# Kernel tuning notes

Measured on AMD Instinct MI355X. Metric: run time of the kernel, lower is better.

Reference implementation:

```python
import jax, jax.numpy as jnp
import numpy as np

N_NODES = 50000
N_EDGES = 600000
D_FEAT = 128
OUT_DIM = 128


def setup_inputs() -> dict:
    key = jax.random.key(0)
    k1, k2, k3, k4 = jax.random.split(key, 4)
    self_feat = jax.random.normal(k1, (N_NODES, D_FEAT), dtype=jnp.float32)
    nbr_feat = jax.random.normal(k2, (N_EDGES, D_FEAT), dtype=jnp.float32)
    relation_src_indices = jax.random.randint(k3, (N_EDGES,), 0, N_NODES, dtype=jnp.int32)
    # Dense(output_dim, use_bias=False), input dim = 2*D_FEAT due to concat
    W = jax.random.normal(k4, (2 * D_FEAT, OUT_DIM), dtype=jnp.float32) * (1.0 / np.sqrt(2 * D_FEAT))
    return {"self_feat": self_feat, "nbr_feat": nbr_feat,
            "relation_src_indices": relation_src_indices, "W": W}


def reference(self_feat, nbr_feat, relation_src_indices, W):
    num_nodes = self_feat.shape[0]
    # unsorted_segment_mean: sum / count, 0 for empty segments (TF semantics)
    seg_sum = jax.ops.segment_sum(nbr_feat, relation_src_indices, num_segments=num_nodes)
    counts = jax.ops.segment_sum(jnp.ones((nbr_feat.shape[0],), dtype=nbr_feat.dtype),
                                 relation_src_indices, num_segments=num_nodes)
    agg = jnp.where(counts[:, None] > 0, seg_sum / jnp.maximum(counts[:, None], 1.0), 0.0)
    out = jnp.concatenate([self_feat, agg], axis=-1)  # [N, 2*D]
    return out @ W  # [N, OUT_DIM]
```

## Files before the change

### kernel.cpp

```cpp
#include <hip/hip_runtime.h>

#define D 128
#define K2 256
#define CAP 96
#define BM 64

typedef float vfloat4 __attribute__((ext_vector_type(4)));
typedef float f32x4 __attribute__((ext_vector_type(4)));
typedef short bf16x8 __attribute__((ext_vector_type(8)));
typedef unsigned short ushort8 __attribute__((ext_vector_type(8)));
typedef unsigned short ushort4v __attribute__((ext_vector_type(4)));

__device__ __forceinline__ unsigned short f2bf(float f) {
    unsigned int u = __float_as_uint(f);
    u += 0x7fffu + ((u >> 16) & 1u);
    return (unsigned short)(u >> 16);
}
__device__ __forceinline__ float bf2f(unsigned short h) {
    return __uint_as_float((unsigned int)h << 16);
}


__global__ void scatter_hist_kernel(const int* __restrict__ idx, int* __restrict__ cnt,
                                    int* __restrict__ eid, int n) {
    int e = blockIdx.x * 256 + threadIdx.x;
    if (e < n) {
        int node = idx[e];
        int p = atomicAdd(&cnt[node], 1);
        if (p < CAP) eid[(size_t)node * CAP + p] = e;
    }
}


__global__ __launch_bounds__(256) void wsplit_kernel(const float* __restrict__ W,
                                                     unsigned short* __restrict__ wh,
                                                     unsigned short* __restrict__ wl) {
    const int k = threadIdx.x;
    const int n = blockIdx.x;
    float x = W[(size_t)k * D + n];
    unsigned short h = f2bf(x);
    float lo = x - bf2f(h);
    wh[(size_t)n * K2 + k] = h;
    wl[(size_t)n * K2 + k] = f2bf(lo);
}


__global__ __launch_bounds__(256) void fused_kernel(const float* __restrict__ self,
                                                    const float* __restrict__ nbr,
                                                    const int* __restrict__ cnt,
                                                    const int* __restrict__ eid,
                                                    const unsigned short* __restrict__ whT,
                                                    const unsigned short* __restrict__ wlT,
                                                    float* __restrict__ out, int nNodes) {
    __shared__ alignas(16) unsigned short AhAll[BM * D];
    __shared__ alignas(16) unsigned short AlAll[BM * D];
    __shared__ alignas(16) unsigned short AhS[BM * 32];
    __shared__ alignas(16) unsigned short AlS[BM * 32];

    const int t = threadIdx.x;
    const int m_base = blockIdx.x * BM;

    {
        const int w = t >> 6;
        const int l = t & 63;
        const int h = l >> 5;
        const int li = l & 31;
        const vfloat4* __restrict__ rows = (const vfloat4*)nbr;
        for (int i = 0; i < 16; ++i) {
            const int r = w * 16 + i;
            const int node = m_base + r;
            if (node >= nNodes) continue;
            const int c0 = cnt[node];
            const int c = (c0 > CAP) ? CAP : c0;
            const int* __restrict__ eb = eid + (size_t)node * CAP;
            vfloat4 acc = {0.f, 0.f, 0.f, 0.f};
            int j = 0;
            for (; j + 8 <= c; j += 8) {
                int e0 = eb[j + 0 + h];
                int e1 = eb[j + 2 + h];
                int e2 = eb[j + 4 + h];
                int e3 = eb[j + 6 + h];
                vfloat4 v0 = __builtin_nontemporal_load(rows + (size_t)e0 * 32 + li);
                vfloat4 v1 = __builtin_nontemporal_load(rows + (size_t)e1 * 32 + li);
                vfloat4 v2 = __builtin_nontemporal_load(rows + (size_t)e2 * 32 + li);
                vfloat4 v3 = __builtin_nontemporal_load(rows + (size_t)e3 * 32 + li);
                acc += (v0 + v1) + (v2 + v3);
            }
            if (j + 4 <= c) {
                int e0 = eb[j + 0 + h];
                int e1 = eb[j + 2 + h];
                vfloat4 v0 = __builtin_nontemporal_load(rows + (size_t)e0 * 32 + li);
                vfloat4 v1 = __builtin_nontemporal_load(rows + (size_t)e1 * 32 + li);
                acc += v0 + v1;
                j += 4;
            }
            for (; j < c; j += 2) {
                int jj = j + h;
                if (jj < c) {
                    int e = eb[jj];
                    vfloat4 v = __builtin_nontemporal_load(rows + (size_t)e * 32 + li);
                    acc += v;
                }
            }
            acc.x += __shfl_xor(acc.x, 32);
            acc.y += __shfl_xor(acc.y, 32);
            acc.z += __shfl_xor(acc.z, 32);
            acc.w += __shfl_xor(acc.w, 32);
            if (h == 0) {
                float inv = (c > 0) ? 1.0f / (float)c : 0.0f;
                vfloat4 o = acc * inv;
                float vv[4] = {o.x, o.y, o.z, o.w};
                ushort4v hv, lv;
#pragma unroll
                for (int q = 0; q < 4; ++q) {
                    unsigned short hh = f2bf(vv[q]);
                    hv[q] = hh;
                    lv[q] = f2bf(vv[q] - bf2f(hh));
                }
                const int sp = ((li >> 1) ^ (r & 7)) * 8 + (li & 1) * 4;
                *(ushort4v*)&AhAll[r * D + sp] = hv;
                *(ushort4v*)&AlAll[r * D + sp] = lv;
            }
        }
    }
    __syncthreads();

    const int sr = t >> 2;
    const int sq = t & 3;
    const int sp = sq ^ ((sr >> 1) & 3);
    int gr = m_base + sr;
    if (gr >= nNodes) gr = nNodes - 1;

    const int wid = t >> 6;
    const int l = t & 63;
    const int wm = (wid >> 1) << 5;
    const int wn = (wid & 1) << 6;
    const int lr = l & 15;
    const int g = l >> 4;
    const int slot = g ^ ((lr >> 1) & 3);

    f32x4 acc[2][4];
#pragma unroll
    for (int i = 0; i < 2; ++i)
#pragma unroll
        for (int j = 0; j < 4; ++j) acc[i][j] = (f32x4){0.f, 0.f, 0.f, 0.f};

    for (int k0 = 0; k0 < D; k0 += 32) {
        const float* p = self + (size_t)gr * D + k0 + sq * 8;
        vfloat4 v0 = ((const vfloat4*)p)[0];
        vfloat4 v1 = ((const vfloat4*)p)[1];
        float xs[8] = {v0.x, v0.y, v0.z, v0.w, v1.x, v1.y, v1.z, v1.w};
        ushort8 hv, lv;
#pragma unroll
        for (int i = 0; i < 8; ++i) {
            unsigned short hh = f2bf(xs[i]);
            hv[i] = hh;
            lv[i] = f2bf(xs[i] - bf2f(hh));
        }
        *(ushort8*)&AhS[sr * 32 + sp * 8] = hv;
        *(ushort8*)&AlS[sr * 32 + sp * 8] = lv;
        __syncthreads();

        bf16x8 bh[4], bl[4], ah[2], al[2];
#pragma unroll
        for (int nf = 0; nf < 4; ++nf) {
            size_t boff = (size_t)(wn + nf * 16 + lr) * K2 + k0 + g * 8;
            bh[nf] = *(const bf16x8*)(whT + boff);
            bl[nf] = *(const bf16x8*)(wlT + boff);
        }
#pragma unroll
        for (int mf = 0; mf < 2; ++mf) {
            int row = wm + mf * 16 + lr;
            ah[mf] = *(const bf16x8*)&AhS[row * 32 + slot * 8];
            al[mf] = *(const bf16x8*)&AlS[row * 32 + slot * 8];
        }
#pragma unroll
        for (int mf = 0; mf < 2; ++mf)
#pragma unroll
            for (int nf = 0; nf < 4; ++nf)
                acc[mf][nf] = __builtin_amdgcn_mfma_f32_16x16x32_bf16(ah[mf], bh[nf], acc[mf][nf], 0, 0, 0);
#pragma unroll
        for (int mf = 0; mf < 2; ++mf)
#pragma unroll
            for (int nf = 0; nf < 4; ++nf)
                acc[mf][nf] = __builtin_amdgcn_mfma_f32_16x16x32_bf16(ah[mf], bl[nf], acc[mf][nf], 0, 0, 0);
#pragma unroll
        for (int mf = 0; mf < 2; ++mf)
#pragma unroll
            for (int nf = 0; nf < 4; ++nf)
                acc[mf][nf] = __builtin_amdgcn_mfma_f32_16x16x32_bf16(al[mf], bh[nf], acc[mf][nf], 0, 0, 0);
        __syncthreads();
    }

    for (int k0 = D; k0 < K2; k0 += 32) {
        bf16x8 bh[4], bl[4], ah[2], al[2];
#pragma unroll
        for (int nf = 0; nf < 4; ++nf) {
            size_t boff = (size_t)(wn + nf * 16 + lr) * K2 + k0 + g * 8;
            bh[nf] = *(const bf16x8*)(whT + boff);
            bl[nf] = *(const bf16x8*)(wlT + boff);
        }
        const int s_log = ((k0 - D) >> 3) + g;
#pragma unroll
        for (int mf = 0; mf < 2; ++mf) {
            int row = wm + mf * 16 + lr;
            int s_phys = s_log ^ (row & 7);
            ah[mf] = *(const bf16x8*)&AhAll[row * D + s_phys * 8];
            al[mf] = *(const bf16x8*)&AlAll[row * D + s_phys * 8];
        }
#pragma unroll
        for (int mf = 0; mf < 2; ++mf)
#pragma unroll
            for (int nf = 0; nf < 4; ++nf)
                acc[mf][nf] = __builtin_amdgcn_mfma_f32_16x16x32_bf16(ah[mf], bh[nf], acc[mf][nf], 0, 0, 0);
#pragma unroll
        for (int mf = 0; mf < 2; ++mf)
#pragma unroll
            for (int nf = 0; nf < 4; ++nf)
                acc[mf][nf] = __builtin_amdgcn_mfma_f32_16x16x32_bf16(ah[mf], bl[nf], acc[mf][nf], 0, 0, 0);
#pragma unroll
        for (int mf = 0; mf < 2; ++mf)
#pragma unroll
            for (int nf = 0; nf < 4; ++nf)
                acc[mf][nf] = __builtin_amdgcn_mfma_f32_16x16x32_bf16(al[mf], bh[nf], acc[mf][nf], 0, 0, 0);
    }

#pragma unroll
    for (int mf = 0; mf < 2; ++mf) {
#pragma unroll
        for (int rr = 0; rr < 4; ++rr) {
            int m = m_base + wm + mf * 16 + g * 4 + rr;
            if (m < nNodes) {
                float* po = out + (size_t)m * D + wn + lr;
#pragma unroll
                for (int nf = 0; nf < 4; ++nf) po[nf * 16] = acc[mf][nf][rr];
            }
        }
    }
}


extern "C" void kernel_launch(void* const* d_in, const int* in_sizes, int n_in,
                              void* d_out, int out_size, void* d_ws, size_t ws_size,
                              hipStream_t stream) {
    const float* self = (const float*)d_in[0];
    const float* nbr = (const float*)d_in[1];
    const int* idx = (const int*)d_in[2];
    const float* W = (const float*)d_in[3];
    float* out = (float*)d_out;

    const int nNodes = in_sizes[0] / D;
    const int nEdges = in_sizes[2];

    int* cnt = (int*)d_ws;
    int* eid = cnt + nNodes;
    size_t csr_bytes = (size_t)nNodes * (1 + CAP) * sizeof(int);
    csr_bytes = (csr_bytes + 15) & ~(size_t)15;
    unsigned short* whT = (unsigned short*)((char*)d_ws + csr_bytes);
    unsigned short* wlT = whT + (size_t)D * K2;

    hipMemsetAsync(cnt, 0, (size_t)nNodes * sizeof(int), stream);
    wsplit_kernel<<<D, K2, 0, stream>>>(W, whT, wlT);
    scatter_hist_kernel<<<(nEdges + 255) / 256, 256, 0, stream>>>(idx, cnt, eid, nEdges);
    fused_kernel<<<(nNodes + BM - 1) / BM, 256, 0, stream>>>(self, nbr, cnt, eid, whT, wlT,
                                                             out, nNodes);
}
```

Before: 500.9 us.

## Fuse count zeroing into W-split kernel and load self features directly into MFMA registers

Replaces the separate memset with a loop inside the weight-split kernel that zeroes the count array, removing one launch. In the self-feature GEMM phase, each lane now loads its own fp32 self rows from global memory and converts them to bf16 hi/lo fragments in registers. This drops the shared staging buffers and the two barriers per k-step. Self rows are now read redundantly by the two N-halves of warps, and the index load is marked nontemporal.

```diff
diff --git a/kernel.cpp b/kernel.cpp
--- a/kernel.cpp
+++ b/kernel.cpp
@@ -21,20 +21,10 @@
 }
 
 
-__global__ void scatter_hist_kernel(const int* __restrict__ idx, int* __restrict__ cnt,
-                                    int* __restrict__ eid, int n) {
-    int e = blockIdx.x * 256 + threadIdx.x;
-    if (e < n) {
-        int node = idx[e];
-        int p = atomicAdd(&cnt[node], 1);
-        if (p < CAP) eid[(size_t)node * CAP + p] = e;
-    }
-}
-
-
-__global__ __launch_bounds__(256) void wsplit_kernel(const float* __restrict__ W,
-                                                     unsigned short* __restrict__ wh,
-                                                     unsigned short* __restrict__ wl) {
+__global__ __launch_bounds__(256) void prep_kernel(const float* __restrict__ W,
+                                                   unsigned short* __restrict__ wh,
+                                                   unsigned short* __restrict__ wl,
+                                                   int* __restrict__ cnt, int nNodes) {
     const int k = threadIdx.x;
     const int n = blockIdx.x;
     float x = W[(size_t)k * D + n];
@@ -42,6 +32,18 @@
     float lo = x - bf2f(h);
     wh[(size_t)n * K2 + k] = h;
     wl[(size_t)n * K2 + k] = f2bf(lo);
+    for (int i = blockIdx.x * 256 + threadIdx.x; i < nNodes; i += 128 * 256) cnt[i] = 0;
+}
+
+
+__global__ void scatter_hist_kernel(const int* __restrict__ idx, int* __restrict__ cnt,
+                                    int* __restrict__ eid, int n) {
+    int e = blockIdx.x * 256 + threadIdx.x;
+    if (e < n) {
+        int node = __builtin_nontemporal_load(idx + e);
+        int p = atomicAdd(&cnt[node], 1);
+        if (p < CAP) eid[(size_t)node * CAP + p] = e;
+    }
 }
 
 
@@ -54,8 +56,6 @@
                                                     float* __restrict__ out, int nNodes) {
     __shared__ alignas(16) unsigned short AhAll[BM * D];
     __shared__ alignas(16) unsigned short AlAll[BM * D];
-    __shared__ alignas(16) unsigned short AhS[BM * 32];
-    __shared__ alignas(16) unsigned short AlS[BM * 32];
 
     const int t = threadIdx.x;
     const int m_base = blockIdx.x * BM;
@@ -125,19 +125,12 @@
     }
     __syncthreads();
 
-    const int sr = t >> 2;
-    const int sq = t & 3;
-    const int sp = sq ^ ((sr >> 1) & 3);
-    int gr = m_base + sr;
-    if (gr >= nNodes) gr = nNodes - 1;
-
     const int wid = t >> 6;
     const int l = t & 63;
     const int wm = (wid >> 1) << 5;
     const int wn = (wid & 1) << 6;
     const int lr = l & 15;
     const int g = l >> 4;
-    const int slot = g ^ ((lr >> 1) & 3);
 
     f32x4 acc[2][4];
 #pragma unroll
@@ -145,22 +138,15 @@
 #pragma unroll
         for (int j = 0; j < 4; ++j) acc[i][j] = (f32x4){0.f, 0.f, 0.f, 0.f};
 
+    const float* selfRow[2];
+#pragma unroll
+    for (int mf = 0; mf < 2; ++mf) {
+        int row = m_base + wm + mf * 16 + lr;
+        if (row >= nNodes) row = nNodes - 1;
+        selfRow[mf] = self + (size_t)row * D + g * 8;
+    }
+
     for (int k0 = 0; k0 < D; k0 += 32) {
-        const float* p = self + (size_t)gr * D + k0 + sq * 8;
-        vfloat4 v0 = ((const vfloat4*)p)[0];
-        vfloat4 v1 = ((const vfloat4*)p)[1];
-        float xs[8] = {v0.x, v0.y, v0.z, v0.w, v1.x, v1.y, v1.z, v1.w};
-        ushort8 hv, lv;
-#pragma unroll
-        for (int i = 0; i < 8; ++i) {
-            unsigned short hh = f2bf(xs[i]);
-            hv[i] = hh;
-            lv[i] = f2bf(xs[i] - bf2f(hh));
-        }
-        *(ushort8*)&AhS[sr * 32 + sp * 8] = hv;
-        *(ushort8*)&AlS[sr * 32 + sp * 8] = lv;
-        __syncthreads();
-
         bf16x8 bh[4], bl[4], ah[2], al[2];
 #pragma unroll
         for (int nf = 0; nf < 4; ++nf) {
@@ -170,9 +156,19 @@
         }
 #pragma unroll
         for (int mf = 0; mf < 2; ++mf) {
-            int row = wm + mf * 16 + lr;
-            ah[mf] = *(const bf16x8*)&AhS[row * 32 + slot * 8];
-            al[mf] = *(const bf16x8*)&AlS[row * 32 + slot * 8];
+            const float* p = selfRow[mf] + k0;
+            vfloat4 v0 = ((const vfloat4*)p)[0];
+            vfloat4 v1 = ((const vfloat4*)p)[1];
+            float xs[8] = {v0.x, v0.y, v0.z, v0.w, v1.x, v1.y, v1.z, v1.w};
+            ushort8 hv, lv;
+#pragma unroll
+            for (int q = 0; q < 8; ++q) {
+                unsigned short hh = f2bf(xs[q]);
+                hv[q] = hh;
+                lv[q] = f2bf(xs[q] - bf2f(hh));
+            }
+            ah[mf] = (bf16x8)hv;
+            al[mf] = (bf16x8)lv;
         }
 #pragma unroll
         for (int mf = 0; mf < 2; ++mf)
@@ -189,7 +185,6 @@
 #pragma unroll
             for (int nf = 0; nf < 4; ++nf)
                 acc[mf][nf] = __builtin_amdgcn_mfma_f32_16x16x32_bf16(al[mf], bh[nf], acc[mf][nf], 0, 0, 0);
-        __syncthreads();
     }
 
     for (int k0 = D; k0 < K2; k0 += 32) {
@@ -259,8 +254,7 @@
     unsigned short* whT = (unsigned short*)((char*)d_ws + csr_bytes);
     unsigned short* wlT = whT + (size_t)D * K2;
 
-    hipMemsetAsync(cnt, 0, (size_t)nNodes * sizeof(int), stream);
-    wsplit_kernel<<<D, K2, 0, stream>>>(W, whT, wlT);
+    prep_kernel<<<D, K2, 0, stream>>>(W, whT, wlT, cnt, nNodes);
     scatter_hist_kernel<<<(nEdges + 255) / 256, 256, 0, stream>>>(idx, cnt, eid, nEdges);
     fused_kernel<<<(nNodes + BM - 1) / BM, 256, 0, stream>>>(self, nbr, cnt, eid, whT, wlT,
                                                              out, nNodes);
```

Result: slower. 540.9 us (+8.0%).
